# Optimization experiments

Measured on AMD Instinct MI355X. Metric: run time of the kernel, lower is better.

Reference implementation:

```python
import jax, jax.numpy as jnp
import numpy as np

MAX_SH_DEGREE = 3
NUM_BASES = (MAX_SH_DEGREE + 1) ** 2  # 16


def eval_sh_bases_fast(dirs):
    """SH bases up to degree 3 for unit directions [..., 3] -> [..., 16].
    Matches gsplat's _eval_sh_bases_fast constants/order."""
    x, y, z = dirs[..., 0], dirs[..., 1], dirs[..., 2]
    z2 = z * z
    fTmp0B = -1.092548430592079 * z
    fC1 = x * x - y * y
    fS1 = 2.0 * x * y
    fTmp0C = -2.285228997322329 * z2 + 0.4570457994644658
    fTmp1B = 1.445305721320277 * z
    fC2 = x * fC1 - y * fS1
    fS2 = x * fS1 + y * fC1
    ones = jnp.full_like(x, 0.2820947917738781)
    return jnp.stack([
        ones,
        -0.48860251190292 * y,
        0.48860251190292 * z,
        -0.48860251190292 * x,
        0.5462742152960395 * fS1,
        fTmp0B * y,
        0.9461746957575601 * z2 - 0.3153915652525201,
        fTmp0B * x,
        0.5462742152960395 * fC1,
        -0.5900435899266435 * fS2,
        fTmp1B * fS1,
        fTmp0C * y,
        z * (1.865881662950577 * z2 - 1.119528997770346),
        fTmp0C * x,
        fTmp1B * fC1,
        -0.5900435899266435 * fC2,
    ], axis=-1)


def setup_inputs() -> dict:
    key = jax.random.key(0)
    ks = jax.random.split(key, 10)
    C, N, F, E, W = 4, 250000, 32, 16, 128
    D_IN = E + F + NUM_BASES  # 64
    return {
        "features": jax.random.normal(ks[0], (N, F), jnp.float32),
        "dirs": jax.random.normal(ks[1], (C, N, 3), jnp.float32),
        "embed_table": jax.random.normal(ks[2], (1000, E), jnp.float32) * 0.1,
        "W0": jax.random.normal(ks[3], (D_IN, W), jnp.float32) / np.sqrt(D_IN),
        "b0": jax.random.normal(ks[4], (W,), jnp.float32) * 0.01,
        "W1": jax.random.normal(ks[5], (W, W), jnp.float32) / np.sqrt(W),
        "b1": jax.random.normal(ks[6], (W,), jnp.float32) * 0.01,
        "W2": jax.random.normal(ks[7], (W, 3), jnp.float32) / np.sqrt(W),
        "b2": jax.random.normal(ks[8], (3,), jnp.float32) * 0.01,
        "embed_ids": jax.random.randint(ks[9], (C,), 0, 1000, jnp.int64 if jax.config.jax_enable_x64 else jnp.int32),
        "sh_degree": 3,
    }


def reference(features, dirs, embed_table, W0, b0, W1, b1, W2, b2, embed_ids, sh_degree):
    C, N = dirs.shape[:2]
    E = embed_table.shape[1]
    F_dim = features.shape[1]
    # camera embeddings broadcast over splats
    emb = embed_table[embed_ids]                                   # [C, E]
    emb = jnp.broadcast_to(emb[:, None, :], (C, N, E))
    feats = jnp.broadcast_to(features[None, :, :], (C, N, F_dim))
    # F.normalize(dirs, dim=-1): divide by norm clamped at eps=1e-12
    norm = jnp.linalg.norm(dirs, axis=-1, keepdims=True)
    nd = dirs / jnp.maximum(norm, 1e-12)
    nb_use = (sh_degree + 1) ** 2  # static python int
    sh = eval_sh_bases_fast(nd)                                    # [C, N, 16]
    if nb_use < NUM_BASES:  # zero bases beyond requested degree
        mask = (jnp.arange(NUM_BASES) < nb_use).astype(sh.dtype)
        sh = sh * mask
    x = jnp.concatenate([emb, feats, sh], axis=-1)                 # [C, N, 64]
    h = jax.nn.relu(x @ W0 + b0)
    h = jax.nn.relu(h @ W1 + b1)
    return h @ W2 + b2                                             # [C, N, 3]
```

## Files before the change

### kernel.cpp

```cpp
#include <hip/hip_runtime.h>
#include <cstdint>
#include <cstddef>

typedef _Float16 half8 __attribute__((ext_vector_type(8)));
typedef __fp16 fp16x2 __attribute__((ext_vector_type(2)));
typedef float floatx16 __attribute__((ext_vector_type(16)));


__global__ void vdc_prep_kernel(const float* __restrict__ W0,
                                const float* __restrict__ W1,
                                const float* __restrict__ W2,
                                const float* __restrict__ b0,
                                const float* __restrict__ b1,
                                const float* __restrict__ b2,
                                const float* __restrict__ emb_tab,
                                const int* __restrict__ embed_ids,
                                int C,
                                _Float16* __restrict__ ws) {
    int i = blockIdx.x * 256 + threadIdx.x;
    int w0end = C * 8192;
    int w1end = w0end + 18432;
    int w2end = w1end + 4608;
    float v = 0.0f;
    if (i < w0end) {
        int c = i >> 13, r = i & 8191;
        int ci = r >> 9, l = (r >> 3) & 63, ii = r & 7;
        int mt = ci >> 2, ks = ci & 3;
        int j  = mt * 32 + (l & 31);
        int kk = ks * 16 + (l >> 5) * 8 + ii;
        if (kk < 48) v = W0[(16 + kk) * 128 + j];
        else if (kk == 48) {
            int id = embed_ids[c];
            v = b0[j];
            #pragma unroll
            for (int e = 0; e < 16; ++e)
                v += emb_tab[(size_t)id * 16 + e] * W0[e * 128 + j];
        }
        ws[i] = (_Float16)v;
    } else if (i < w1end) {
        int r = i - w0end;
        int ci = r >> 9, l = (r >> 3) & 63, ii = r & 7;
        int mt = ci / 9, ks = ci - mt * 9;
        int j  = mt * 32 + (l & 31);
        int kk = ks * 16 + (l >> 5) * 8 + ii;
        if (kk < 128) v = W1[kk * 128 + j];
        else if (kk == 128) v = b1[j];
        ws[i] = (_Float16)v;
    } else if (i < w2end) {
        int r = i - w1end;
        int ks = r >> 9, l = (r >> 3) & 63, ii = r & 7;
        int o  = l & 31;
        int kk = ks * 16 + (l >> 5) * 8 + ii;
        if (o < 3) {
            if (kk < 128) v = W2[kk * 3 + o];
            else if (kk == 128) v = b2[o];
        }
        ws[i] = (_Float16)v;
    }
}

union U4 { unsigned u[4]; half8 h; };

__device__ __forceinline__ unsigned pkr(float a, float b) {
    union { fp16x2 h; unsigned u; } x;
    x.h = __builtin_amdgcn_cvt_pkrtz(a, b);
    return x.u;
}

__device__ __forceinline__ void transition(const floatx16& a, int hl,
                                           half8& lo, half8& hi) {
    unsigned p0 = pkr(fmaxf(a[0],  0.f), fmaxf(a[1],  0.f));
    unsigned p1 = pkr(fmaxf(a[2],  0.f), fmaxf(a[3],  0.f));
    unsigned p2 = pkr(fmaxf(a[4],  0.f), fmaxf(a[5],  0.f));
    unsigned p3 = pkr(fmaxf(a[6],  0.f), fmaxf(a[7],  0.f));
    unsigned p4 = pkr(fmaxf(a[8],  0.f), fmaxf(a[9],  0.f));
    unsigned p5 = pkr(fmaxf(a[10], 0.f), fmaxf(a[11], 0.f));
    unsigned p6 = pkr(fmaxf(a[12], 0.f), fmaxf(a[13], 0.f));
    unsigned p7 = pkr(fmaxf(a[14], 0.f), fmaxf(a[15], 0.f));
    unsigned r0 = __shfl_xor(hl ? p0 : p2, 32);
    unsigned r1 = __shfl_xor(hl ? p1 : p3, 32);
    unsigned r2 = __shfl_xor(hl ? p4 : p6, 32);
    unsigned r3 = __shfl_xor(hl ? p5 : p7, 32);
    U4 L, H;
    L.u[0] = hl ? r0 : p0;
    L.u[1] = hl ? r1 : p1;
    L.u[2] = hl ? p2 : r0;
    L.u[3] = hl ? p3 : r1;
    H.u[0] = hl ? r2 : p4;
    H.u[1] = hl ? r3 : p5;
    H.u[2] = hl ? p6 : r2;
    H.u[3] = hl ? p7 : r3;
    lo = L.h; hi = H.h;
}

#define MFMA(a, b, c) __builtin_amdgcn_mfma_f32_32x32x16_f16((a), (b), (c), 0, 0, 0)

__global__ __launch_bounds__(512, 4) void vdc_mlp_kernel(
    const float* __restrict__ feats,
    const float* __restrict__ dirs,
    const int* __restrict__ sh_deg_p,
    const _Float16* __restrict__ ws,
    float* __restrict__ out,
    int N, int C)
{
    __shared__ uint4 arena[3904];
    char* lds = (char*)arena;

    const int tid   = threadIdx.x;
    const int c     = blockIdx.y;
    const int w     = tid >> 6;
    const int lane  = tid & 63;
    const int ln    = lane & 31;
    const int hl    = lane >> 5;
    const int base  = blockIdx.x * 256 + w * 32;

    {
        const uint4* srcA = (const uint4*)(ws + (size_t)c * 8192);
        const uint4* srcB = (const uint4*)(ws + (size_t)C * 8192);
        #pragma unroll
        for (int it = 0; it < 8; ++it) {
            int idx = it * 512 + tid;
            if (idx < 3904)
                arena[idx] = (idx < 1024) ? srcA[idx] : srcB[idx - 1024];
        }
    }

    half8 bx0, bx1, bx2, bbias;
    {
        U4 ub;
        ub.u[0] = hl ? 0u : 0x00003C00u;
        ub.u[1] = 0u; ub.u[2] = 0u; ub.u[3] = 0u;
        bbias = ub.h;
    }
    {
        int n = base + ln; if (n >= N) n = N - 1;
        const float* fp = feats + (size_t)n * 32 + hl * 8;
        float4 f0 = *(const float4*)(fp);
        float4 f1 = *(const float4*)(fp + 4);
        float4 f2 = *(const float4*)(fp + 16);
        float4 f3 = *(const float4*)(fp + 20);
        U4 u0, u1;
        u0.u[0] = pkr(f0.x, f0.y); u0.u[1] = pkr(f0.z, f0.w);
        u0.u[2] = pkr(f1.x, f1.y); u0.u[3] = pkr(f1.z, f1.w);
        u1.u[0] = pkr(f2.x, f2.y); u1.u[1] = pkr(f2.z, f2.w);
        u1.u[2] = pkr(f3.x, f3.y); u1.u[3] = pkr(f3.z, f3.w);
        bx0 = u0.h; bx1 = u1.h;

        const float* dp = dirs + ((size_t)c * N + n) * 3;
        float dx = dp[0], dy = dp[1], dz = dp[2];
        float nrm = sqrtf(dx * dx + dy * dy + dz * dz);
        float inv = 1.0f / fmaxf(nrm, 1e-12f);
        float x = dx * inv, y = dy * inv, z = dz * inv;

        float z2     = z * z;
        float fTmp0B = -1.092548430592079f * z;
        float fC1    = x * x - y * y;
        float fS1    = 2.0f * x * y;
        float fTmp0C = -2.285228997322329f * z2 + 0.4570457994644658f;
        float fTmp1B = 1.445305721320277f * z;
        float fC2    = x * fC1 - y * fS1;
        float fS2    = x * fS1 + y * fC1;

        float sh[16];
        sh[0]  = 0.2820947917738781f;
        sh[1]  = -0.48860251190292f * y;
        sh[2]  = 0.48860251190292f * z;
        sh[3]  = -0.48860251190292f * x;
        sh[4]  = 0.5462742152960395f * fS1;
        sh[5]  = fTmp0B * y;
        sh[6]  = 0.9461746957575601f * z2 - 0.3153915652525201f;
        sh[7]  = fTmp0B * x;
        sh[8]  = 0.5462742152960395f * fC1;
        sh[9]  = -0.5900435899266435f * fS2;
        sh[10] = fTmp1B * fS1;
        sh[11] = fTmp0C * y;
        sh[12] = z * (1.865881662950577f * z2 - 1.119528997770346f);
        sh[13] = fTmp0C * x;
        sh[14] = fTmp1B * fC1;
        sh[15] = -0.5900435899266435f * fC2;

        int deg = sh_deg_p[0];
        int nbu = (deg + 1) * (deg + 1);
        #pragma unroll
        for (int i = 0; i < 16; ++i) if (i >= nbu) sh[i] = 0.0f;

        float s[8];
        #pragma unroll
        for (int i = 0; i < 8; ++i) s[i] = hl ? sh[8 + i] : sh[i];
        U4 u2;
        u2.u[0] = pkr(s[0], s[1]); u2.u[1] = pkr(s[2], s[3]);
        u2.u[2] = pkr(s[4], s[5]); u2.u[3] = pkr(s[6], s[7]);
        bx2 = u2.h;
    }

    __syncthreads();

    const char* fr = lds + lane * 16;

    half8 hx[8];
    #pragma unroll
    for (int mt = 0; mt < 4; ++mt) {
        half8 a0 = *(const half8*)(fr + (mt * 4 + 0) * 1024);
        half8 a1 = *(const half8*)(fr + (mt * 4 + 1) * 1024);
        half8 a2 = *(const half8*)(fr + (mt * 4 + 2) * 1024);
        half8 a3 = *(const half8*)(fr + (mt * 4 + 3) * 1024);
        floatx16 acc;
        #pragma unroll
        for (int r = 0; r < 16; ++r) acc[r] = 0.0f;
        acc = MFMA(a0, bx0, acc);
        acc = MFMA(a1, bx1, acc);
        acc = MFMA(a2, bx2, acc);
        acc = MFMA(a3, bbias, acc);
        transition(acc, hl, hx[2 * mt], hx[2 * mt + 1]);
    }

    floatx16 acc3;
    #pragma unroll
    for (int r = 0; r < 16; ++r) acc3[r] = 0.0f;

    #pragma unroll
    for (int mt = 0; mt < 4; ++mt) {
        const char* ap = fr + 16384 + mt * 9 * 1024;
        floatx16 acc;
        #pragma unroll
        for (int r = 0; r < 16; ++r) acc[r] = 0.0f;
        #pragma unroll
        for (int ks = 0; ks < 8; ++ks) {
            half8 a = *(const half8*)(ap + ks * 1024);
            acc = MFMA(a, hx[ks], acc);
        }
        half8 ab = *(const half8*)(ap + 8 * 1024);
        acc = MFMA(ab, bbias, acc);

        half8 g0, g1;
        transition(acc, hl, g0, g1);

        half8 w2a = *(const half8*)(fr + 53248 + (2 * mt + 0) * 1024);
        half8 w2b = *(const half8*)(fr + 53248 + (2 * mt + 1) * 1024);
        acc3 = MFMA(w2a, g0, acc3);
        acc3 = MFMA(w2b, g1, acc3);
    }
    {
        half8 ab = *(const half8*)(fr + 53248 + 8 * 1024);
        acc3 = MFMA(ab, bbias, acc3);
    }

    if (hl == 0) {
        int nn = base + ln;
        if (nn < N) {
            float* op = out + ((size_t)c * N + nn) * 3;
            op[0] = acc3[0];
            op[1] = acc3[1];
            op[2] = acc3[2];
        }
    }
}

extern "C" void kernel_launch(void* const* d_in, const int* in_sizes, int n_in,
                              void* d_out, int out_size, void* d_ws, size_t ws_size,
                              hipStream_t stream) {
    const float* feats   = (const float*)d_in[0];
    const float* dirs    = (const float*)d_in[1];
    const float* emb_tab = (const float*)d_in[2];
    const float* W0      = (const float*)d_in[3];
    const float* b0      = (const float*)d_in[4];
    const float* W1      = (const float*)d_in[5];
    const float* b1      = (const float*)d_in[6];
    const float* W2      = (const float*)d_in[7];
    const float* b2      = (const float*)d_in[8];
    const int*   eids    = (const int*)d_in[9];
    const int*   shd     = (const int*)d_in[10];
    float* outp          = (float*)d_out;

    int N = in_sizes[0] / 32;
    int C = in_sizes[9];

    _Float16* wsh = (_Float16*)d_ws;

    int ws_elems = C * 8192 + 23040;
    vdc_prep_kernel<<<(ws_elems + 255) / 256, 256, 0, stream>>>(
        W0, W1, W2, b0, b1, b2, emb_tab, eids, C, wsh);

    dim3 grid((N + 255) / 256, C);
    vdc_mlp_kernel<<<grid, 512, 0, stream>>>(
        feats, dirs, shd, wsh, outp, N, C);
}
```

Baseline: 165.0 us.

## Process two 32-point tiles per wave to reuse LDS weight fragments

Each wave now handles 64 points, as two 32-column MFMA tiles, instead of 32. Every weight fragment loaded from LDS feeds two MFMAs. Blocks shrink to 256 threads, so each block still covers 256 points and the per-block weight staging is spread over fewer threads. The aim is to halve LDS reads per MFMA and give each wave two independent accumulator chains for latency hiding, at the cost of higher register pressure and fewer waves per CU.

```diff
diff --git a/kernel.cpp b/kernel.cpp
--- a/kernel.cpp
+++ b/kernel.cpp
@@ -67,6 +67,13 @@
     return x.u;
 }
 
+__device__ __forceinline__ floatx16 zero16() {
+    floatx16 z;
+    #pragma unroll
+    for (int r = 0; r < 16; ++r) z[r] = 0.0f;
+    return z;
+}
+
 __device__ __forceinline__ void transition(const floatx16& a, int hl,
                                            half8& lo, half8& hi) {
     unsigned p0 = pkr(fmaxf(a[0],  0.f), fmaxf(a[1],  0.f));
@@ -93,9 +100,124 @@
     lo = L.h; hi = H.h;
 }
 
+__device__ __forceinline__ void build_bfrags(
+    const float* __restrict__ feats, const float* __restrict__ dirs,
+    size_t cN, int n, int hl, int nbu,
+    half8& o0, half8& o1, half8& o2)
+{
+    const float* fp = feats + (size_t)n * 32 + hl * 8;
+    float4 f0 = *(const float4*)(fp);
+    float4 f1 = *(const float4*)(fp + 4);
+    float4 f2 = *(const float4*)(fp + 16);
+    float4 f3 = *(const float4*)(fp + 20);
+    U4 u0, u1;
+    u0.u[0] = pkr(f0.x, f0.y); u0.u[1] = pkr(f0.z, f0.w);
+    u0.u[2] = pkr(f1.x, f1.y); u0.u[3] = pkr(f1.z, f1.w);
+    u1.u[0] = pkr(f2.x, f2.y); u1.u[1] = pkr(f2.z, f2.w);
+    u1.u[2] = pkr(f3.x, f3.y); u1.u[3] = pkr(f3.z, f3.w);
+    o0 = u0.h; o1 = u1.h;
+
+    const float* dp = dirs + (cN + n) * 3;
+    float dx = dp[0], dy = dp[1], dz = dp[2];
+    float nrm = sqrtf(dx * dx + dy * dy + dz * dz);
+    float inv = 1.0f / fmaxf(nrm, 1e-12f);
+    float x = dx * inv, y = dy * inv, z = dz * inv;
+
+    float z2     = z * z;
+    float fTmp0B = -1.092548430592079f * z;
+    float fC1    = x * x - y * y;
+    float fS1    = 2.0f * x * y;
+    float fTmp0C = -2.285228997322329f * z2 + 0.4570457994644658f;
+    float fTmp1B = 1.445305721320277f * z;
+    float fC2    = x * fC1 - y * fS1;
+    float fS2    = x * fS1 + y * fC1;
+
+    float sh[16];
+    sh[0]  = 0.2820947917738781f;
+    sh[1]  = -0.48860251190292f * y;
+    sh[2]  = 0.48860251190292f * z;
+    sh[3]  = -0.48860251190292f * x;
+    sh[4]  = 0.5462742152960395f * fS1;
+    sh[5]  = fTmp0B * y;
+    sh[6]  = 0.9461746957575601f * z2 - 0.3153915652525201f;
+    sh[7]  = fTmp0B * x;
+    sh[8]  = 0.5462742152960395f * fC1;
+    sh[9]  = -0.5900435899266435f * fS2;
+    sh[10] = fTmp1B * fS1;
+    sh[11] = fTmp0C * y;
+    sh[12] = z * (1.865881662950577f * z2 - 1.119528997770346f);
+    sh[13] = fTmp0C * x;
+    sh[14] = fTmp1B * fC1;
+    sh[15] = -0.5900435899266435f * fC2;
+    #pragma unroll
+    for (int i = 0; i < 16; ++i) if (i >= nbu) sh[i] = 0.0f;
+
+    float s0 = hl ? sh[8]  : sh[0];
+    float s1 = hl ? sh[9]  : sh[1];
+    float s2 = hl ? sh[10] : sh[2];
+    float s3 = hl ? sh[11] : sh[3];
+    float s4 = hl ? sh[12] : sh[4];
+    float s5 = hl ? sh[13] : sh[5];
+    float s6 = hl ? sh[14] : sh[6];
+    float s7 = hl ? sh[15] : sh[7];
+    U4 u2;
+    u2.u[0] = pkr(s0, s1); u2.u[1] = pkr(s2, s3);
+    u2.u[2] = pkr(s4, s5); u2.u[3] = pkr(s6, s7);
+    o2 = u2.h;
+}
+
 #define MFMA(a, b, c) __builtin_amdgcn_mfma_f32_32x32x16_f16((a), (b), (c), 0, 0, 0)
-
-__global__ __launch_bounds__(512, 4) void vdc_mlp_kernel(
+#define LDF(off) (*(const half8*)(fr + (off)))
+
+#define L0_MT(MT, HA0, HA1, HB0, HB1)                                    \
+    do {                                                                 \
+        half8 a0 = LDF(((MT) * 4 + 0) * 1024);                           \
+        half8 a1 = LDF(((MT) * 4 + 1) * 1024);                           \
+        half8 a2 = LDF(((MT) * 4 + 2) * 1024);                           \
+        half8 a3 = LDF(((MT) * 4 + 3) * 1024);                           \
+        floatx16 acc = zero16();                                         \
+        acc = MFMA(a0, ax0, acc); acc = MFMA(a1, ax1, acc);              \
+        acc = MFMA(a2, ax2, acc); acc = MFMA(a3, bbias, acc);            \
+        transition(acc, hl, HA0, HA1);                                   \
+        acc = zero16();                                                  \
+        acc = MFMA(a0, bx0, acc); acc = MFMA(a1, bx1, acc);              \
+        acc = MFMA(a2, bx2, acc); acc = MFMA(a3, bbias, acc);            \
+        transition(acc, hl, HB0, HB1);                                   \
+    } while (0)
+
+#define L1_MT(MT)                                                        \
+    do {                                                                 \
+        half8 q0 = LDF(16384 + ((MT) * 9 + 0) * 1024);                   \
+        half8 q1 = LDF(16384 + ((MT) * 9 + 1) * 1024);                   \
+        half8 q2 = LDF(16384 + ((MT) * 9 + 2) * 1024);                   \
+        half8 q3 = LDF(16384 + ((MT) * 9 + 3) * 1024);                   \
+        half8 q4 = LDF(16384 + ((MT) * 9 + 4) * 1024);                   \
+        half8 q5 = LDF(16384 + ((MT) * 9 + 5) * 1024);                   \
+        half8 q6 = LDF(16384 + ((MT) * 9 + 6) * 1024);                   \
+        half8 q7 = LDF(16384 + ((MT) * 9 + 7) * 1024);                   \
+        half8 q8 = LDF(16384 + ((MT) * 9 + 8) * 1024);                   \
+        half8 w2a = LDF(53248 + (2 * (MT) + 0) * 1024);                  \
+        half8 w2b = LDF(53248 + (2 * (MT) + 1) * 1024);                  \
+        floatx16 acc = zero16();                                         \
+        acc = MFMA(q0, ha0, acc); acc = MFMA(q1, ha1, acc);              \
+        acc = MFMA(q2, ha2, acc); acc = MFMA(q3, ha3, acc);              \
+        acc = MFMA(q4, ha4, acc); acc = MFMA(q5, ha5, acc);              \
+        acc = MFMA(q6, ha6, acc); acc = MFMA(q7, ha7, acc);              \
+        acc = MFMA(q8, bbias, acc);                                      \
+        half8 g0, g1;                                                    \
+        transition(acc, hl, g0, g1);                                     \
+        acc3a = MFMA(w2a, g0, acc3a); acc3a = MFMA(w2b, g1, acc3a);      \
+        acc = zero16();                                                  \
+        acc = MFMA(q0, hb0, acc); acc = MFMA(q1, hb1, acc);              \
+        acc = MFMA(q2, hb2, acc); acc = MFMA(q3, hb3, acc);              \
+        acc = MFMA(q4, hb4, acc); acc = MFMA(q5, hb5, acc);              \
+        acc = MFMA(q6, hb6, acc); acc = MFMA(q7, hb7, acc);              \
+        acc = MFMA(q8, bbias, acc);                                      \
+        transition(acc, hl, g0, g1);                                     \
+        acc3b = MFMA(w2a, g0, acc3b); acc3b = MFMA(w2b, g1, acc3b);      \
+    } while (0)
+
+__global__ __launch_bounds__(256, 2) void vdc_mlp_kernel(
     const float* __restrict__ feats,
     const float* __restrict__ dirs,
     const int* __restrict__ sh_deg_p,
@@ -112,146 +234,72 @@
     const int lane  = tid & 63;
     const int ln    = lane & 31;
     const int hl    = lane >> 5;
-    const int base  = blockIdx.x * 256 + w * 32;
+    const int base  = blockIdx.x * 256 + w * 64;
 
     {
         const uint4* srcA = (const uint4*)(ws + (size_t)c * 8192);
         const uint4* srcB = (const uint4*)(ws + (size_t)C * 8192);
         #pragma unroll
-        for (int it = 0; it < 8; ++it) {
-            int idx = it * 512 + tid;
-            if (idx < 3904)
-                arena[idx] = (idx < 1024) ? srcA[idx] : srcB[idx - 1024];
-        }
-    }
-
-    half8 bx0, bx1, bx2, bbias;
+        for (int it = 0; it < 15; ++it) {
+            int idx = it * 256 + tid;
+            arena[idx] = (idx < 1024) ? srcA[idx] : srcB[idx - 1024];
+        }
+        int idx = 15 * 256 + tid;
+        if (idx < 3904) arena[idx] = srcB[idx - 1024];
+    }
+
+    half8 bbias;
     {
         U4 ub;
         ub.u[0] = hl ? 0u : 0x00003C00u;
         ub.u[1] = 0u; ub.u[2] = 0u; ub.u[3] = 0u;
         bbias = ub.h;
     }
+    int deg = sh_deg_p[0];
+    int nbu = (deg + 1) * (deg + 1);
+    int na = base + ln;      if (na >= N) na = N - 1;
+    int nb = base + 32 + ln; if (nb >= N) nb = N - 1;
+    half8 ax0, ax1, ax2, bx0, bx1, bx2;
+    build_bfrags(feats, dirs, (size_t)c * N, na, hl, nbu, ax0, ax1, ax2);
+    build_bfrags(feats, dirs, (size_t)c * N, nb, hl, nbu, bx0, bx1, bx2);
+
+    __syncthreads();
+
+    const char* fr = lds + lane * 16;
+
+    half8 ha0, ha1, ha2, ha3, ha4, ha5, ha6, ha7;
+    half8 hb0, hb1, hb2, hb3, hb4, hb5, hb6, hb7;
+    L0_MT(0, ha0, ha1, hb0, hb1);
+    L0_MT(1, ha2, ha3, hb2, hb3);
+    L0_MT(2, ha4, ha5, hb4, hb5);
+    L0_MT(3, ha6, ha7, hb6, hb7);
+
+    floatx16 acc3a = zero16();
+    floatx16 acc3b = zero16();
+    L1_MT(0);
+    L1_MT(1);
+    L1_MT(2);
+    L1_MT(3);
     {
-        int n = base + ln; if (n >= N) n = N - 1;
-        const float* fp = feats + (size_t)n * 32 + hl * 8;
-        float4 f0 = *(const float4*)(fp);
-        float4 f1 = *(const float4*)(fp + 4);
-        float4 f2 = *(const float4*)(fp + 16);
-        float4 f3 = *(const float4*)(fp + 20);
-        U4 u0, u1;
-        u0.u[0] = pkr(f0.x, f0.y); u0.u[1] = pkr(f0.z, f0.w);
-        u0.u[2] = pkr(f1.x, f1.y); u0.u[3] = pkr(f1.z, f1.w);
-        u1.u[0] = pkr(f2.x, f2.y); u1.u[1] = pkr(f2.z, f2.w);
-        u1.u[2] = pkr(f3.x, f3.y); u1.u[3] = pkr(f3.z, f3.w);
-        bx0 = u0.h; bx1 = u1.h;
-
-        const float* dp = dirs + ((size_t)c * N + n) * 3;
-        float dx = dp[0], dy = dp[1], dz = dp[2];
-        float nrm = sqrtf(dx * dx + dy * dy + dz * dz);
-        float inv = 1.0f / fmaxf(nrm, 1e-12f);
-        float x = dx * inv, y = dy * inv, z = dz * inv;
-
-        float z2     = z * z;
-        float fTmp0B = -1.092548430592079f * z;
-        float fC1    = x * x - y * y;
-        float fS1    = 2.0f * x * y;
-        float fTmp0C = -2.285228997322329f * z2 + 0.4570457994644658f;
-        float fTmp1B = 1.445305721320277f * z;
-        float fC2    = x * fC1 - y * fS1;
-        float fS2    = x * fS1 + y * fC1;
-
-        float sh[16];
-        sh[0]  = 0.2820947917738781f;
-        sh[1]  = -0.48860251190292f * y;
-        sh[2]  = 0.48860251190292f * z;
-        sh[3]  = -0.48860251190292f * x;
-        sh[4]  = 0.5462742152960395f * fS1;
-        sh[5]  = fTmp0B * y;
-        sh[6]  = 0.9461746957575601f * z2 - 0.3153915652525201f;
-        sh[7]  = fTmp0B * x;
-        sh[8]  = 0.5462742152960395f * fC1;
-        sh[9]  = -0.5900435899266435f * fS2;
-        sh[10] = fTmp1B * fS1;
-        sh[11] = fTmp0C * y;
-        sh[12] = z * (1.865881662950577f * z2 - 1.119528997770346f);
-        sh[13] = fTmp0C * x;
-        sh[14] = fTmp1B * fC1;
-        sh[15] = -0.5900435899266435f * fC2;
-
-        int deg = sh_deg_p[0];
-        int nbu = (deg + 1) * (deg + 1);
-        #pragma unroll
-        for (int i = 0; i < 16; ++i) if (i >= nbu) sh[i] = 0.0f;
-
-        float s[8];
-        #pragma unroll
-        for (int i = 0; i < 8; ++i) s[i] = hl ? sh[8 + i] : sh[i];
-        U4 u2;
-        u2.u[0] = pkr(s[0], s[1]); u2.u[1] = pkr(s[2], s[3]);
-        u2.u[2] = pkr(s[4], s[5]); u2.u[3] = pkr(s[6], s[7]);
-        bx2 = u2.h;
-    }
-
-    __syncthreads();
-
-    const char* fr = lds + lane * 16;
-
-    half8 hx[8];
-    #pragma unroll
-    for (int mt = 0; mt < 4; ++mt) {
-        half8 a0 = *(const half8*)(fr + (mt * 4 + 0) * 1024);
-        half8 a1 = *(const half8*)(fr + (mt * 4 + 1) * 1024);
-        half8 a2 = *(const half8*)(fr + (mt * 4 + 2) * 1024);
-        half8 a3 = *(const half8*)(fr + (mt * 4 + 3) * 1024);
-        floatx16 acc;
-        #pragma unroll
-        for (int r = 0; r < 16; ++r) acc[r] = 0.0f;
-        acc = MFMA(a0, bx0, acc);
-        acc = MFMA(a1, bx1, acc);
-        acc = MFMA(a2, bx2, acc);
-        acc = MFMA(a3, bbias, acc);
-        transition(acc, hl, hx[2 * mt], hx[2 * mt + 1]);
-    }
-
-    floatx16 acc3;
-    #pragma unroll
-    for (int r = 0; r < 16; ++r) acc3[r] = 0.0f;
-
-    #pragma unroll
-    for (int mt = 0; mt < 4; ++mt) {
-        const char* ap = fr + 16384 + mt * 9 * 1024;
-        floatx16 acc;
-        #pragma unroll
-        for (int r = 0; r < 16; ++r) acc[r] = 0.0f;
-        #pragma unroll
-        for (int ks = 0; ks < 8; ++ks) {
-            half8 a = *(const half8*)(ap + ks * 1024);
-            acc = MFMA(a, hx[ks], acc);
-        }
-        half8 ab = *(const half8*)(ap + 8 * 1024);
-        acc = MFMA(ab, bbias, acc);
-
-        half8 g0, g1;
-        transition(acc, hl, g0, g1);
-
-        half8 w2a = *(const half8*)(fr + 53248 + (2 * mt + 0) * 1024);
-        half8 w2b = *(const half8*)(fr + 53248 + (2 * mt + 1) * 1024);
-        acc3 = MFMA(w2a, g0, acc3);
-        acc3 = MFMA(w2b, g1, acc3);
-    }
-    {
-        half8 ab = *(const half8*)(fr + 53248 + 8 * 1024);
-        acc3 = MFMA(ab, bbias, acc3);
+        half8 ab = LDF(53248 + 8 * 1024);
+        acc3a = MFMA(ab, bbias, acc3a);
+        acc3b = MFMA(ab, bbias, acc3b);
     }
 
     if (hl == 0) {
         int nn = base + ln;
         if (nn < N) {
             float* op = out + ((size_t)c * N + nn) * 3;
-            op[0] = acc3[0];
-            op[1] = acc3[1];
-            op[2] = acc3[2];
+            op[0] = acc3a[0];
+            op[1] = acc3a[1];
+            op[2] = acc3a[2];
+        }
+        nn = base + 32 + ln;
+        if (nn < N) {
+            float* op = out + ((size_t)c * N + nn) * 3;
+            op[0] = acc3b[0];
+            op[1] = acc3b[1];
+            op[2] = acc3b[2];
         }
     }
 }
@@ -282,6 +330,6 @@
         W0, W1, W2, b0, b1, b2, emb_tab, eids, C, wsh);
 
     dim3 grid((N + 255) / 256, C);
-    vdc_mlp_kernel<<<grid, 512, 0, stream>>>(
+    vdc_mlp_kernel<<<grid, 256, 0, stream>>>(
         feats, dirs, shd, wsh, outp, N, C);
 }
```

After: 160.5 us. -2.8%, faster.
